# Kernel tuning notes

Hardware: AMD Instinct MI355X
Metric: run time of the kernel (lower is better)

Reference implementation:

```python
import jax, jax.numpy as jnp
import numpy as np

D_MODEL = 1024
NUM_HEADS = 16
HEAD_DIM = D_MODEL // NUM_HEADS
WINDOW = 16
DILATION = 3
SCALE = HEAD_DIM ** -0.5


def _linear(x, W, b):
    # torch nn.Linear: y = x @ W.T + b, W: [out, in]
    return x @ W.T + b


def _chunk_attention(x, Wq, bq, Wk, bk, Wv, bv, chunk):
    B, L, D = x.shape
    pad = (-L) % chunk
    if pad:
        x = jnp.pad(x, ((0, 0), (0, pad), (0, 0)))
    Lp = L + pad
    nC = Lp // chunk
    xr = x.reshape(B * nC, chunk, D)  # [BC, c, D]

    def heads(t):
        return t.reshape(B * nC, chunk, NUM_HEADS, HEAD_DIM).transpose(0, 2, 1, 3)

    q = heads(_linear(xr, Wq, bq))  # [BC, H, c, hd]
    k = heads(_linear(xr, Wk, bk))
    v = heads(_linear(xr, Wv, bv))
    attn = jax.nn.softmax(jnp.einsum('bhqd,bhkd->bhqk', q, k) * SCALE, axis=-1)
    out = jnp.einsum('bhqk,bhkd->bhqd', attn, v)  # [BC, H, c, hd]
    out = out.transpose(0, 2, 1, 3).reshape(B, Lp, D)
    return out[:, :L, :]


def setup_inputs() -> dict:
    key = jax.random.key(0)
    ks = jax.random.split(key, 9)
    s = 1.0 / np.sqrt(D_MODEL)
    x = jax.random.normal(ks[0], (4, 4096, D_MODEL), dtype=jnp.float32)
    def lin(kw, kb):
        W = jax.random.uniform(kw, (D_MODEL, D_MODEL), minval=-s, maxval=s, dtype=jnp.float32)
        b = jax.random.uniform(kb, (D_MODEL,), minval=-s, maxval=s, dtype=jnp.float32)
        return W, b
    Wq, bq = lin(ks[1], ks[2])
    Wk, bk = lin(ks[3], ks[4])
    Wv, bv = lin(ks[5], ks[6])
    Wo, bo = lin(ks[7], ks[8])
    return {"x": x, "Wq": Wq, "bq": bq, "Wk": Wk, "bk": bk,
            "Wv": Wv, "bv": bv, "Wo": Wo, "bo": bo}


def reference(x, Wq, bq, Wk, bk, Wv, bv, Wo, bo):
    B, L, D = x.shape
    # local windowed attention
    local_out = _chunk_attention(x, Wq, bq, Wk, bk, Wv, bv, WINDOW)
    # dilated (atrous) attention: stride-DILATION interleave via reshape/permute
    pad = (-L) % DILATION
    x_pad = jnp.pad(x, ((0, 0), (0, pad), (0, 0))) if pad else x
    Lp = L + pad
    xv = x_pad.reshape(B, Lp // DILATION, DILATION, D).transpose(0, 2, 1, 3)
    x_atrous = xv.reshape(B * DILATION, Lp // DILATION, D)
    a = _chunk_attention(x_atrous, Wq, bq, Wk, bk, Wv, bv, WINDOW)
    a = a.reshape(B, DILATION, Lp // DILATION, D).transpose(0, 2, 1, 3).reshape(B, Lp, D)
    atrous_out = a[:, :L, :]
    return _linear(local_out + atrous_out, Wo, bo)
```

## Files before the change

kernel.cpp:

```cpp
#include <hip/hip_runtime.h>
#include <hip/hip_bf16.h>
#include <stdint.h>

typedef unsigned short ushort_t;
typedef __attribute__((ext_vector_type(8))) short bf16x8;
typedef __attribute__((ext_vector_type(4))) float f32x4;

__device__ __forceinline__ ushort_t f2bf(float f) {
    uint32_t u = __builtin_bit_cast(uint32_t, f);
    u += 0x7FFF + ((u >> 16) & 1);
    return (ushort_t)(u >> 16);
}
__device__ __forceinline__ float bf2f(ushort_t h) {
    return __builtin_bit_cast(float, (uint32_t)h << 16);
}

__device__ __forceinline__ f32x4 mfma16(bf16x8 a, bf16x8 b, f32x4 c) {
    return __builtin_amdgcn_mfma_f32_16x16x32_bf16(a, b, c, 0, 0, 0);
}

#define GLL(g, l) __builtin_amdgcn_global_load_lds(                              \
    (const __attribute__((address_space(1))) void*)(g),                          \
    (__attribute__((address_space(3))) void*)(l), 16, 0, 0)

#define CFENCE asm volatile("" ::: "memory")
#define BARRIER do { CFENCE; __builtin_amdgcn_s_barrier(); CFENCE; } while (0)
#define PRIO1 __builtin_amdgcn_s_setprio(1)
#define PRIO0 __builtin_amdgcn_s_setprio(0)
#define VM4 asm volatile("s_waitcnt vmcnt(4)" ::: "memory")
#define VM0 asm volatile("s_waitcnt vmcnt(0)" ::: "memory")


__device__ __forceinline__ void cvt8(const float* s, ushort_t* d) {
    float4 a = ((const float4*)s)[0], b = ((const float4*)s)[1];
    union { bf16x8 v; ushort_t u[8]; } o;
    o.u[0] = f2bf(a.x); o.u[1] = f2bf(a.y); o.u[2] = f2bf(a.z); o.u[3] = f2bf(a.w);
    o.u[4] = f2bf(b.x); o.u[5] = f2bf(b.y); o.u[6] = f2bf(b.z); o.u[7] = f2bf(b.w);
    *(bf16x8*)d = o.v;
}

__global__ __launch_bounds__(256) void cvt_all(
    const float* __restrict__ x,
    const float* __restrict__ Wq, const float* __restrict__ Wk,
    const float* __restrict__ Wv, const float* __restrict__ Wo,
    const float* __restrict__ bq, const float* __restrict__ bk,
    const float* __restrict__ bv,
    ushort_t* __restrict__ xb, ushort_t* __restrict__ wqkv,
    float* __restrict__ bqkv)
{
    const int NX = 16384 * 1024 / 8;
    const int NW = 1024 * 1024 / 8;
    int i = blockIdx.x * 256 + threadIdx.x;
    if (i < NX) {
        cvt8(x + (size_t)i * 8, xb + (size_t)i * 8);
    } else if (i < NX + 4 * NW) {
        int j = i - NX;
        int w = j >> 17, off = j & (NW - 1);
        const float* s = (w == 0) ? Wq : (w == 1) ? Wk : (w == 2) ? Wv : Wo;
        cvt8(s + (size_t)off * 8, wqkv + (size_t)j * 8);
    } else if (i < NX + 4 * NW + 384) {
        int j = i - NX - 4 * NW;
        int w2 = j >> 7, off = j & 127;
        const float* s = (w2 == 0) ? bq : (w2 == 1) ? bk : bv;
        ((float4*)(bqkv + j * 8))[0] = ((const float4*)(s + off * 8))[0];
        ((float4*)(bqkv + j * 8))[1] = ((const float4*)(s + off * 8))[1];
    }
}


#define STGA(bq, kt) { _Pragma("unroll")                                         \
    for (int j = 0; j < 2; ++j) {                                                \
        int idx = j * 512 + tid; int row = idx >> 2, ch = idx & 3;               \
        GLL(A + (size_t)(m0 + row) * 1024 + (kt) * 32 + ((ch ^ (row & 3)) * 8),  \
            (char*)&As[bq][0] + (size_t)idx * 16);                               \
    } }
#define STGB(bq, kt) { _Pragma("unroll")                                         \
    for (int j = 0; j < 2; ++j) {                                                \
        int idx = j * 512 + tid; int row = idx >> 2, ch = idx & 3;               \
        GLL(B + (size_t)(n0 + row) * 1024 + (kt) * 32 + ((ch ^ (row & 3)) * 8),  \
            (char*)&Bs[bq][0] + (size_t)idx * 16);                               \
    } }

#define RD4(dst, bq, mibase) { _Pragma("unroll")                                 \
    for (int q = 0; q < 4; ++q)                                                  \
        dst[q] = *(const bf16x8*)&As[bq][(wm * 128 + ((mibase) + q) * 16 + ln)   \
                                        * 32 + cho]; }
#define RDB(dst, bq) { _Pragma("unroll")                                         \
    for (int q = 0; q < 4; ++q)                                                  \
        dst[q] = *(const bf16x8*)&Bs[bq][(wn * 64 + q * 16 + ln) * 32 + cho]; }

#define MFMA16(mibase, av, bv) { _Pragma("unroll")                               \
    for (int mi = 0; mi < 4; ++mi) _Pragma("unroll")                             \
        for (int ni = 0; ni < 4; ++ni)                                           \
            acc[(mibase) + mi][ni] =                                             \
                mfma16(av[mi], bv[ni], acc[(mibase) + mi][ni]); }

template<int MODE>
__global__ __launch_bounds__(512, 2) void gemm6(
    const ushort_t* __restrict__ A, const ushort_t* __restrict__ B,
    const float* __restrict__ bias, void* __restrict__ outp,
    int M, int NTN)
{
    __shared__ ushort_t As[4][256 * 32];
    __shared__ ushort_t Bs[4][256 * 32];
    const int NK = 32;

    const int bid = blockIdx.x;
    const int nwg = gridDim.x;
    const int q8 = nwg >> 3;
    const int swz = (bid & 7) * q8 + (bid >> 3);
    const int m0 = (swz / NTN) * 256;
    const int n0 = (swz % NTN) * 256;

    const int tid = threadIdx.x;
    const int wave = tid >> 6, lane = tid & 63;
    const int wm = wave >> 2, wn = wave & 3;
    const int lg = lane >> 4, ln = lane & 15;
    const int cho = (lg ^ (ln & 3)) * 8;

    f32x4 acc[8][4];
#pragma unroll
    for (int i2 = 0; i2 < 8; ++i2)
#pragma unroll
        for (int j2 = 0; j2 < 4; ++j2) acc[i2][j2] = (f32x4){0.f, 0.f, 0.f, 0.f};

    STGA(0, 0) STGB(0, 0)
    STGA(1, 1) STGB(1, 1)
    STGA(2, 2) STGB(2, 2)
    VM4;
    BARRIER;

    bf16x8 aE0[4], aE1[4], aO0[4], aO1[4], bE[4], bO[4];
    RD4(aE0, 0, 0) RDB(bE, 0)

    for (int it = 0; it < 16; ++it) {
        const int ke = 2 * it, ko = ke + 1;
        const int ce = (it & 1) << 1, co = ce | 1;
        const int s1 = (ke + 3) & 3;
        const int s2 = ce;
        const bool p1 = (ke + 3 < NK), p2 = (ko + 3 < NK);

        RD4(aE1, ce, 4)
        if (p1) STGA(s1, ke + 3)
        PRIO1; MFMA16(0, aE0, bE) PRIO0;

        RD4(aO0, co, 0) RDB(bO, co)
        if (p1) STGB(s1, ke + 3)
        PRIO1; MFMA16(4, aE1, bE) PRIO0;
        if (p1) { VM4; } else { VM0; }
        BARRIER;

        RD4(aO1, co, 4)
        if (p2) STGA(s2, ko + 3)
        PRIO1; MFMA16(0, aO0, bO) PRIO0;

        if (it + 1 < 16) { RD4(aE0, (ce + 2) & 3, 0) RDB(bE, (ce + 2) & 3) }
        if (p2) STGB(s2, ko + 3)
        PRIO1; MFMA16(4, aO1, bO) PRIO0;
        if (p2) { VM4; } else { VM0; }
        BARRIER;
    }

    float bval[4];
#pragma unroll
    for (int ni = 0; ni < 4; ++ni) bval[ni] = bias[n0 + wn * 64 + ni * 16 + ln];

    if (MODE == 0) {
        ushort_t* obase = (ushort_t*)outp + (size_t)(n0 >> 10) * ((size_t)M * 1024)
                          + (n0 & 1023) + wn * 64 + ln;
#pragma unroll
        for (int mi = 0; mi < 8; ++mi) {
#pragma unroll
            for (int r = 0; r < 4; ++r) {
                int m = m0 + wm * 128 + mi * 16 + lg * 4 + r;
                ushort_t* orow = obase + (size_t)m * 1024;
#pragma unroll
                for (int ni = 0; ni < 4; ++ni)
                    orow[ni * 16] = f2bf(acc[mi][ni][r] + bval[ni]);
            }
        }
    } else {
        float* obase = (float*)outp + n0 + wn * 64 + ln;
#pragma unroll
        for (int mi = 0; mi < 8; ++mi) {
#pragma unroll
            for (int r = 0; r < 4; ++r) {
                int m = m0 + wm * 128 + mi * 16 + lg * 4 + r;
                float* orow = obase + (size_t)m * 1024;
#pragma unroll
                for (int ni = 0; ni < 4; ++ni)
                    orow[ni * 16] = acc[mi][ni][r] + bval[ni];
            }
        }
    }
}


__device__ __forceinline__ bf16x8 bias8(const float* __restrict__ b, int off) {
    float4 f0 = *(const float4*)(b + off);
    float4 f1 = *(const float4*)(b + off + 4);
    union { bf16x8 v; ushort_t u[8]; } o;
    o.u[0] = f2bf(f0.x); o.u[1] = f2bf(f0.y); o.u[2] = f2bf(f0.z); o.u[3] = f2bf(f0.w);
    o.u[4] = f2bf(f1.x); o.u[5] = f2bf(f1.y); o.u[6] = f2bf(f1.z); o.u[7] = f2bf(f1.w);
    return o.v;
}


__global__ __launch_bounds__(256) void attn_local(
    const ushort_t* __restrict__ Q, const ushort_t* __restrict__ K,
    const ushort_t* __restrict__ V, ushort_t* __restrict__ S)
{
    const int wave = threadIdx.x >> 6, lane = threadIdx.x & 63;
    const int unit = blockIdx.x * 4 + wave;
    const int h = unit & 15;
    const int c = unit >> 4;
    const int g = lane >> 4, nn = lane & 15;
    __shared__ ushort_t lds_p[4][16 * 16];
    __shared__ ushort_t vt[4][64 * 16];

    const size_t rowb = (size_t)c * 16;
    size_t aoff = (rowb + nn) * 1024 + h * 64 + g * 8;
    bf16x8 qa0 = *(const bf16x8*)(Q + aoff);
    bf16x8 qa1 = *(const bf16x8*)(Q + aoff + 32);
    bf16x8 kb0 = *(const bf16x8*)(K + aoff);
    bf16x8 kb1 = *(const bf16x8*)(K + aoff + 32);

#pragma unroll
    for (int it = 0; it < 2; ++it) {
        int u = it * 64 + lane;
        int n = u >> 3, cc = u & 7;
        bf16x8 vv = *(const bf16x8*)(V + (rowb + n) * 1024 + h * 64 + cc * 8);
        union { bf16x8 v; ushort_t u8[8]; } vu; vu.v = vv;
#pragma unroll
        for (int j = 0; j < 8; ++j) vt[wave][(cc * 8 + j) * 16 + n] = vu.u8[j];
    }

    f32x4 sc = {0.f, 0.f, 0.f, 0.f};
    sc = mfma16(qa0, kb0, sc);
    sc = mfma16(qa1, kb1, sc);

#pragma unroll
    for (int r = 0; r < 4; ++r) {
        float s = sc[r] * 0.125f;
        float mx = s;
#pragma unroll
        for (int off = 1; off < 16; off <<= 1) mx = fmaxf(mx, __shfl_xor(mx, off, 64));
        float e = __expf(s - mx);
        float sm = e;
#pragma unroll
        for (int off = 1; off < 16; off <<= 1) sm += __shfl_xor(sm, off, 64);
        lds_p[wave][(g * 4 + r) * 16 + nn] = f2bf(e / sm);
    }
    CFENCE;

    bf16x8 zero8 = {};
    bf16x8 pa = (g < 2) ? *(const bf16x8*)&lds_p[wave][nn * 16 + g * 8] : zero8;
#pragma unroll
    for (int dt = 0; dt < 4; ++dt) {
        bf16x8 vb = (g < 2) ? *(const bf16x8*)&vt[wave][(dt * 16 + nn) * 16 + g * 8] : zero8;
        f32x4 o = mfma16(pa, vb, (f32x4){0.f, 0.f, 0.f, 0.f});
#pragma unroll
        for (int r = 0; r < 4; ++r) {
            size_t orow = rowb + g * 4 + r;
            S[orow * 1024 + h * 64 + dt * 16 + nn] = f2bf(o[r]);
        }
    }
}


__global__ __launch_bounds__(256) void attn_atrous(
    const ushort_t* __restrict__ Q, const ushort_t* __restrict__ K,
    const ushort_t* __restrict__ V,
    const float* __restrict__ bq, const float* __restrict__ bk,
    const float* __restrict__ bv, ushort_t* __restrict__ S)
{
    const int wave = threadIdx.x >> 6, lane = threadIdx.x & 63;
    const int unit = blockIdx.x * 4 + wave;
    const int h = unit & 15;
    const int tmp = unit >> 4;
    const int c = tmp % 86;
    const int sidx = tmp / 86;
    const int b = sidx / 3, dil = sidx % 3;
    const int g = lane >> 4, nn = lane & 15;
    __shared__ ushort_t lds_p[4][16 * 16];
    __shared__ ushort_t vt[4][64 * 16];

    const int dof = h * 64 + g * 8;
    const int p_n = 3 * (c * 16 + nn) + dil;
    bf16x8 qa0, qa1, kb0, kb1;
    if (p_n < 4096) {
        size_t o = ((size_t)b * 4096 + p_n) * 1024 + dof;
        qa0 = *(const bf16x8*)(Q + o);
        qa1 = *(const bf16x8*)(Q + o + 32);
        kb0 = *(const bf16x8*)(K + o);
        kb1 = *(const bf16x8*)(K + o + 32);
    } else {
        qa0 = bias8(bq, dof); qa1 = bias8(bq, dof + 32);
        kb0 = bias8(bk, dof); kb1 = bias8(bk, dof + 32);
    }

#pragma unroll
    for (int it = 0; it < 2; ++it) {
        int u = it * 64 + lane;
        int n = u >> 3, cc = u & 7;
        int p_v = 3 * (c * 16 + n) + dil;
        bf16x8 vv = (p_v < 4096)
            ? *(const bf16x8*)(V + ((size_t)b * 4096 + p_v) * 1024 + h * 64 + cc * 8)
            : bias8(bv, h * 64 + cc * 8);
        union { bf16x8 v; ushort_t u8[8]; } vu; vu.v = vv;
#pragma unroll
        for (int j = 0; j < 8; ++j) vt[wave][(cc * 8 + j) * 16 + n] = vu.u8[j];
    }

    f32x4 sc = {0.f, 0.f, 0.f, 0.f};
    sc = mfma16(qa0, kb0, sc);
    sc = mfma16(qa1, kb1, sc);

#pragma unroll
    for (int r = 0; r < 4; ++r) {
        float s = sc[r] * 0.125f;
        float mx = s;
#pragma unroll
        for (int off = 1; off < 16; off <<= 1) mx = fmaxf(mx, __shfl_xor(mx, off, 64));
        float e = __expf(s - mx);
        float sm = e;
#pragma unroll
        for (int off = 1; off < 16; off <<= 1) sm += __shfl_xor(sm, off, 64);
        lds_p[wave][(g * 4 + r) * 16 + nn] = f2bf(e / sm);
    }
    CFENCE;

    bf16x8 zero8 = {};
    bf16x8 pa = (g < 2) ? *(const bf16x8*)&lds_p[wave][nn * 16 + g * 8] : zero8;
#pragma unroll
    for (int dt = 0; dt < 4; ++dt) {
        bf16x8 vb = (g < 2) ? *(const bf16x8*)&vt[wave][(dt * 16 + nn) * 16 + g * 8] : zero8;
        f32x4 o = mfma16(pa, vb, (f32x4){0.f, 0.f, 0.f, 0.f});
#pragma unroll
        for (int r = 0; r < 4; ++r) {
            int p_q = 3 * (c * 16 + g * 4 + r) + dil;
            if (p_q < 4096) {
                size_t off = ((size_t)b * 4096 + p_q) * 1024 + h * 64 + dt * 16 + nn;
                S[off] = f2bf(bf2f(S[off]) + o[r]);
            }
        }
    }
}


extern "C" void kernel_launch(void* const* d_in, const int* in_sizes, int n_in,
                              void* d_out, int out_size, void* d_ws, size_t ws_size,
                              hipStream_t stream)
{
    const float* x  = (const float*)d_in[0];
    const float* Wq = (const float*)d_in[1];
    const float* bq = (const float*)d_in[2];
    const float* Wk = (const float*)d_in[3];
    const float* bk = (const float*)d_in[4];
    const float* Wv = (const float*)d_in[5];
    const float* bv = (const float*)d_in[6];
    const float* Wo = (const float*)d_in[7];
    const float* bo = (const float*)d_in[8];
    float* out = (float*)d_out;

    const size_t NT = 16384;
    ushort_t* xb   = (ushort_t*)d_ws;
    ushort_t* wqkv = xb + NT * 1024;
    ushort_t* wo   = wqkv + 3 * 1024 * 1024;
    ushort_t* Qb   = wo + 1024 * 1024;
    ushort_t* Kb   = Qb + NT * 1024;
    ushort_t* Vb   = Kb + NT * 1024;
    ushort_t* Sb   = Vb + NT * 1024;
    float*    bqkv = (float*)(Sb + NT * 1024);

    const int total_units = 2097152 + 4 * 131072 + 384;
    cvt_all<<<(total_units + 255) / 256, 256, 0, stream>>>(
        x, Wq, Wk, Wv, Wo, bq, bk, bv, xb, wqkv, bqkv);

    gemm6<0><<<768, 512, 0, stream>>>(xb, wqkv, bqkv, (void*)Qb, (int)NT, 12);

    attn_local <<<4096, 256, 0, stream>>>(Qb, Kb, Vb, Sb);
    attn_atrous<<<4128, 256, 0, stream>>>(Qb, Kb, Vb, bq, bk, bv, Sb);

    gemm6<1><<<256, 512, 0, stream>>>(Sb, wo, bo, (void*)out, (int)NT, 4);
}
```

Baseline: 344.9 us.

## Rework GEMM to K=64 double-buffered pipeline and fuse local+atrous attention bands

The GEMM moves from 32-wide K tiles with four stages to 64-wide K tiles with two buffers and an 8-chunk XOR swizzle. The loop is split into four phases, each loading one quarter of the next tile, and the launch bound drops to one block per CU. The two attention kernels are merged into one band kernel: each 48-token band computes its three local chunks and three dilated chunks together and sums them in LDS before a single bf16 store. This removes the read-modify-write of S and one launch. The risks are lower GEMM occupancy, more barriers per iteration, and fewer attention blocks that each loop over four heads with syncthreads.

```diff
diff --git a/kernel.cpp b/kernel.cpp
--- a/kernel.cpp
+++ b/kernel.cpp
@@ -27,7 +27,8 @@
 #define BARRIER do { CFENCE; __builtin_amdgcn_s_barrier(); CFENCE; } while (0)
 #define PRIO1 __builtin_amdgcn_s_setprio(1)
 #define PRIO0 __builtin_amdgcn_s_setprio(0)
-#define VM4 asm volatile("s_waitcnt vmcnt(4)" ::: "memory")
+#define LGKM0 asm volatile("s_waitcnt lgkmcnt(0)" ::: "memory")
+#define VM2 asm volatile("s_waitcnt vmcnt(2)" ::: "memory")
 #define VM0 asm volatile("s_waitcnt vmcnt(0)" ::: "memory")
 
 
@@ -68,42 +69,35 @@
 }
 
 
-#define STGA(bq, kt) { _Pragma("unroll")                                         \
+#define STG7(P, rb, dst, kt) { _Pragma("unroll")                                 \
     for (int j = 0; j < 2; ++j) {                                                \
-        int idx = j * 512 + tid; int row = idx >> 2, ch = idx & 3;               \
-        GLL(A + (size_t)(m0 + row) * 1024 + (kt) * 32 + ((ch ^ (row & 3)) * 8),  \
-            (char*)&As[bq][0] + (size_t)idx * 16);                               \
+        int idx = j * 512 + tid; int row = idx >> 3, ch = idx & 7;               \
+        GLL(P + (size_t)((rb) + row) * 1024 + (kt) * 64 + ((ch ^ (row & 7)) * 8),\
+            (char*)(dst) + (size_t)idx * 16);                                    \
     } }
-#define STGB(bq, kt) { _Pragma("unroll")                                         \
-    for (int j = 0; j < 2; ++j) {                                                \
-        int idx = j * 512 + tid; int row = idx >> 2, ch = idx & 3;               \
-        GLL(B + (size_t)(n0 + row) * 1024 + (kt) * 32 + ((ch ^ (row & 3)) * 8),  \
-            (char*)&Bs[bq][0] + (size_t)idx * 16);                               \
-    } }
-
-#define RD4(dst, bq, mibase) { _Pragma("unroll")                                 \
+
+#define RDA(dst, base, kki) { _Pragma("unroll")                                  \
     for (int q = 0; q < 4; ++q)                                                  \
-        dst[q] = *(const bf16x8*)&As[bq][(wm * 128 + ((mibase) + q) * 16 + ln)   \
-                                        * 32 + cho]; }
-#define RDB(dst, bq) { _Pragma("unroll")                                         \
+        dst[q] = *(const bf16x8*)&Ad[((base) + q) * 16 * 64 + ln * 64 + chA[kki]]; }
+#define RDB(kki) { _Pragma("unroll")                                             \
     for (int q = 0; q < 4; ++q)                                                  \
-        dst[q] = *(const bf16x8*)&Bs[bq][(wn * 64 + q * 16 + ln) * 32 + cho]; }
-
-#define MFMA16(mibase, av, bv) { _Pragma("unroll")                               \
+        bb[q] = *(const bf16x8*)&Bd[(q * 16 + ln) * 64 + chA[kki]]; }
+
+#define MFMA_P(mibase, areg) { _Pragma("unroll")                                 \
     for (int mi = 0; mi < 4; ++mi) _Pragma("unroll")                             \
         for (int ni = 0; ni < 4; ++ni)                                           \
             acc[(mibase) + mi][ni] =                                             \
-                mfma16(av[mi], bv[ni], acc[(mibase) + mi][ni]); }
+                mfma16(areg[mi], bb[ni], acc[(mibase) + mi][ni]); }
 
 template<int MODE>
-__global__ __launch_bounds__(512, 2) void gemm6(
+__global__ __launch_bounds__(512, 1) void gemm7(
     const ushort_t* __restrict__ A, const ushort_t* __restrict__ B,
     const float* __restrict__ bias, void* __restrict__ outp,
     int M, int NTN)
 {
-    __shared__ ushort_t As[4][256 * 32];
-    __shared__ ushort_t Bs[4][256 * 32];
-    const int NK = 32;
+    __shared__ ushort_t As[2][2][128 * 64];
+    __shared__ ushort_t Bs[2][2][128 * 64];
+    const int NK = 16;
 
     const int bid = blockIdx.x;
     const int nwg = gridDim.x;
@@ -116,7 +110,9 @@
     const int wave = tid >> 6, lane = tid & 63;
     const int wm = wave >> 2, wn = wave & 3;
     const int lg = lane >> 4, ln = lane & 15;
-    const int cho = (lg ^ (ln & 3)) * 8;
+    int chA[2];
+    chA[0] = ((0 * 4 + lg) ^ (ln & 7)) * 8;
+    chA[1] = ((1 * 4 + lg) ^ (ln & 7)) * 8;
 
     f32x4 acc[8][4];
 #pragma unroll
@@ -124,40 +120,45 @@
 #pragma unroll
         for (int j2 = 0; j2 < 4; ++j2) acc[i2][j2] = (f32x4){0.f, 0.f, 0.f, 0.f};
 
-    STGA(0, 0) STGB(0, 0)
-    STGA(1, 1) STGB(1, 1)
-    STGA(2, 2) STGB(2, 2)
-    VM4;
+    STG7(A, m0 + 0,   &As[0][0][0], 0)
+    STG7(A, m0 + 128, &As[0][1][0], 0)
+    STG7(B, n0 + 0,   &Bs[0][0][0], 0)
+    STG7(B, n0 + 128, &Bs[0][1][0], 0)
+    STG7(B, n0 + 0,   &Bs[1][0][0], 1)
+    VM2;
     BARRIER;
 
-    bf16x8 aE0[4], aE1[4], aO0[4], aO1[4], bE[4], bO[4];
-    RD4(aE0, 0, 0) RDB(bE, 0)
-
-    for (int it = 0; it < 16; ++it) {
-        const int ke = 2 * it, ko = ke + 1;
-        const int ce = (it & 1) << 1, co = ce | 1;
-        const int s1 = (ke + 3) & 3;
-        const int s2 = ce;
-        const bool p1 = (ke + 3 < NK), p2 = (ko + 3 < NK);
-
-        RD4(aE1, ce, 4)
-        if (p1) STGA(s1, ke + 3)
-        PRIO1; MFMA16(0, aE0, bE) PRIO0;
-
-        RD4(aO0, co, 0) RDB(bO, co)
-        if (p1) STGB(s1, ke + 3)
-        PRIO1; MFMA16(4, aE1, bE) PRIO0;
-        if (p1) { VM4; } else { VM0; }
+    bf16x8 a03[4], a47[4], bb[4];
+    for (int t = 0; t < NK; ++t) {
+        const int d = t & 1, o = d ^ 1;
+        const ushort_t* Ad = &As[d][wm][0];
+        const ushort_t* Bd = &Bs[d][wn >> 1][(wn & 1) * 64 * 64];
+        const bool p1 = (t + 1 < NK), p2 = (t + 2 < NK);
+
+        RDA(a03, 0, 0) RDB(0)
+        if (p1) STG7(B, n0 + 128, &Bs[o][1][0], t + 1)
+        BARRIER; LGKM0;
+        PRIO1; MFMA_P(0, a03) PRIO0;
         BARRIER;
 
-        RD4(aO1, co, 4)
-        if (p2) STGA(s2, ko + 3)
-        PRIO1; MFMA16(0, aO0, bO) PRIO0;
-
-        if (it + 1 < 16) { RD4(aE0, (ce + 2) & 3, 0) RDB(bE, (ce + 2) & 3) }
-        if (p2) STGB(s2, ko + 3)
-        PRIO1; MFMA16(4, aO1, bO) PRIO0;
-        if (p2) { VM4; } else { VM0; }
+        RDA(a47, 4, 0)
+        if (p1) STG7(A, m0 + 0, &As[o][0][0], t + 1)
+        BARRIER; LGKM0;
+        PRIO1; MFMA_P(4, a47) PRIO0;
+        BARRIER;
+
+        RDA(a03, 0, 1) RDB(1)
+        if (p1) STG7(A, m0 + 128, &As[o][1][0], t + 1)
+        BARRIER; LGKM0;
+        PRIO1; MFMA_P(0, a03) PRIO0;
+        BARRIER;
+
+        RDA(a47, 4, 1)
+        if (p2) STG7(B, n0 + 0, &Bs[d][0][0], t + 2)
+        if (p2)      { VM2; }
+        else if (p1) { VM0; }
+        BARRIER; LGKM0;
+        PRIO1; MFMA_P(4, a47) PRIO0;
         BARRIER;
     }
 
@@ -206,144 +207,114 @@
 }
 
 
-__global__ __launch_bounds__(256) void attn_local(
-    const ushort_t* __restrict__ Q, const ushort_t* __restrict__ K,
-    const ushort_t* __restrict__ V, ushort_t* __restrict__ S)
-{
-    const int wave = threadIdx.x >> 6, lane = threadIdx.x & 63;
-    const int unit = blockIdx.x * 4 + wave;
-    const int h = unit & 15;
-    const int c = unit >> 4;
-    const int g = lane >> 4, nn = lane & 15;
-    __shared__ ushort_t lds_p[4][16 * 16];
-    __shared__ ushort_t vt[4][64 * 16];
-
-    const size_t rowb = (size_t)c * 16;
-    size_t aoff = (rowb + nn) * 1024 + h * 64 + g * 8;
-    bf16x8 qa0 = *(const bf16x8*)(Q + aoff);
-    bf16x8 qa1 = *(const bf16x8*)(Q + aoff + 32);
-    bf16x8 kb0 = *(const bf16x8*)(K + aoff);
-    bf16x8 kb1 = *(const bf16x8*)(K + aoff + 32);
-
-#pragma unroll
-    for (int it = 0; it < 2; ++it) {
-        int u = it * 64 + lane;
-        int n = u >> 3, cc = u & 7;
-        bf16x8 vv = *(const bf16x8*)(V + (rowb + n) * 1024 + h * 64 + cc * 8);
-        union { bf16x8 v; ushort_t u8[8]; } vu; vu.v = vv;
-#pragma unroll
-        for (int j = 0; j < 8; ++j) vt[wave][(cc * 8 + j) * 16 + n] = vu.u8[j];
-    }
-
-    f32x4 sc = {0.f, 0.f, 0.f, 0.f};
-    sc = mfma16(qa0, kb0, sc);
-    sc = mfma16(qa1, kb1, sc);
-
-#pragma unroll
-    for (int r = 0; r < 4; ++r) {
-        float s = sc[r] * 0.125f;
-        float mx = s;
-#pragma unroll
-        for (int off = 1; off < 16; off <<= 1) mx = fmaxf(mx, __shfl_xor(mx, off, 64));
-        float e = __expf(s - mx);
-        float sm = e;
-#pragma unroll
-        for (int off = 1; off < 16; off <<= 1) sm += __shfl_xor(sm, off, 64);
-        lds_p[wave][(g * 4 + r) * 16 + nn] = f2bf(e / sm);
-    }
-    CFENCE;
-
-    bf16x8 zero8 = {};
-    bf16x8 pa = (g < 2) ? *(const bf16x8*)&lds_p[wave][nn * 16 + g * 8] : zero8;
-#pragma unroll
-    for (int dt = 0; dt < 4; ++dt) {
-        bf16x8 vb = (g < 2) ? *(const bf16x8*)&vt[wave][(dt * 16 + nn) * 16 + g * 8] : zero8;
-        f32x4 o = mfma16(pa, vb, (f32x4){0.f, 0.f, 0.f, 0.f});
-#pragma unroll
-        for (int r = 0; r < 4; ++r) {
-            size_t orow = rowb + g * 4 + r;
-            S[orow * 1024 + h * 64 + dt * 16 + nn] = f2bf(o[r]);
-        }
-    }
-}
-
-
-__global__ __launch_bounds__(256) void attn_atrous(
+__global__ __launch_bounds__(384) void attn_band(
     const ushort_t* __restrict__ Q, const ushort_t* __restrict__ K,
     const ushort_t* __restrict__ V,
     const float* __restrict__ bq, const float* __restrict__ bk,
     const float* __restrict__ bv, ushort_t* __restrict__ S)
 {
     const int wave = threadIdx.x >> 6, lane = threadIdx.x & 63;
-    const int unit = blockIdx.x * 4 + wave;
-    const int h = unit & 15;
-    const int tmp = unit >> 4;
-    const int c = tmp % 86;
-    const int sidx = tmp / 86;
-    const int b = sidx / 3, dil = sidx % 3;
     const int g = lane >> 4, nn = lane & 15;
-    __shared__ ushort_t lds_p[4][16 * 16];
-    __shared__ ushort_t vt[4][64 * 16];
-
-    const int dof = h * 64 + g * 8;
-    const int p_n = 3 * (c * 16 + nn) + dil;
-    bf16x8 qa0, qa1, kb0, kb1;
-    if (p_n < 4096) {
-        size_t o = ((size_t)b * 4096 + p_n) * 1024 + dof;
-        qa0 = *(const bf16x8*)(Q + o);
-        qa1 = *(const bf16x8*)(Q + o + 32);
-        kb0 = *(const bf16x8*)(K + o);
-        kb1 = *(const bf16x8*)(K + o + 32);
-    } else {
-        qa0 = bias8(bq, dof); qa1 = bias8(bq, dof + 32);
-        kb0 = bias8(bk, dof); kb1 = bias8(bk, dof + 32);
-    }
-
-#pragma unroll
-    for (int it = 0; it < 2; ++it) {
-        int u = it * 64 + lane;
-        int n = u >> 3, cc = u & 7;
-        int p_v = 3 * (c * 16 + n) + dil;
-        bf16x8 vv = (p_v < 4096)
-            ? *(const bf16x8*)(V + ((size_t)b * 4096 + p_v) * 1024 + h * 64 + cc * 8)
-            : bias8(bv, h * 64 + cc * 8);
-        union { bf16x8 v; ushort_t u8[8]; } vu; vu.v = vv;
-#pragma unroll
-        for (int j = 0; j < 8; ++j) vt[wave][(cc * 8 + j) * 16 + n] = vu.u8[j];
-    }
-
-    f32x4 sc = {0.f, 0.f, 0.f, 0.f};
-    sc = mfma16(qa0, kb0, sc);
-    sc = mfma16(qa1, kb1, sc);
-
-#pragma unroll
-    for (int r = 0; r < 4; ++r) {
-        float s = sc[r] * 0.125f;
-        float mx = s;
-#pragma unroll
-        for (int off = 1; off < 16; off <<= 1) mx = fmaxf(mx, __shfl_xor(mx, off, 64));
-        float e = __expf(s - mx);
-        float sm = e;
-#pragma unroll
-        for (int off = 1; off < 16; off <<= 1) sm += __shfl_xor(sm, off, 64);
-        lds_p[wave][(g * 4 + r) * 16 + nn] = f2bf(e / sm);
-    }
-    CFENCE;
-
-    bf16x8 zero8 = {};
-    bf16x8 pa = (g < 2) ? *(const bf16x8*)&lds_p[wave][nn * 16 + g * 8] : zero8;
-#pragma unroll
-    for (int dt = 0; dt < 4; ++dt) {
-        bf16x8 vb = (g < 2) ? *(const bf16x8*)&vt[wave][(dt * 16 + nn) * 16 + g * 8] : zero8;
-        f32x4 o = mfma16(pa, vb, (f32x4){0.f, 0.f, 0.f, 0.f});
+    const int bid = blockIdx.x;
+    const int hq = bid & 3;
+    const int t2 = bid >> 2;
+    const int band = t2 % 86;
+    const int b = t2 / 86;
+
+    __shared__ float Sacc[48 * 64];
+    __shared__ ushort_t vt[6][64 * 16];
+    __shared__ ushort_t lds_p[6][16 * 16];
+
+    const bool is_local = (wave < 3);
+    const int dil = wave - 3;
+    const int tb = band * 48;
+    const size_t batch0 = (size_t)b * 4096;
+
+    for (int hi = 0; hi < 4; ++hi) {
+        const int h = hq * 4 + hi;
+        const int dof = h * 64 + g * 8;
+
+        int tok_n = is_local ? (tb + wave * 16 + nn) : (tb + 3 * nn + dil);
+        bf16x8 qa0, qa1, kb0, kb1;
+        if (is_local || tok_n < 4096) {
+            size_t off = (batch0 + tok_n) * 1024 + dof;
+            qa0 = *(const bf16x8*)(Q + off);
+            qa1 = *(const bf16x8*)(Q + off + 32);
+            kb0 = *(const bf16x8*)(K + off);
+            kb1 = *(const bf16x8*)(K + off + 32);
+        } else {
+            qa0 = bias8(bq, dof); qa1 = bias8(bq, dof + 32);
+            kb0 = bias8(bk, dof); kb1 = bias8(bk, dof + 32);
+        }
+
+#pragma unroll
+        for (int it = 0; it < 2; ++it) {
+            int u = it * 64 + lane;
+            int n = u >> 3, cc = u & 7;
+            int tok_v = is_local ? (tb + wave * 16 + n) : (tb + 3 * n + dil);
+            bf16x8 vv = (is_local || tok_v < 4096)
+                ? *(const bf16x8*)(V + (batch0 + tok_v) * 1024 + h * 64 + cc * 8)
+                : bias8(bv, h * 64 + cc * 8);
+            union { bf16x8 v; ushort_t u8[8]; } vu; vu.v = vv;
+#pragma unroll
+            for (int j = 0; j < 8; ++j) vt[wave][(cc * 8 + j) * 16 + n] = vu.u8[j];
+        }
+
+        f32x4 sc = {0.f, 0.f, 0.f, 0.f};
+        sc = mfma16(qa0, kb0, sc);
+        sc = mfma16(qa1, kb1, sc);
 #pragma unroll
         for (int r = 0; r < 4; ++r) {
-            int p_q = 3 * (c * 16 + g * 4 + r) + dil;
-            if (p_q < 4096) {
-                size_t off = ((size_t)b * 4096 + p_q) * 1024 + h * 64 + dt * 16 + nn;
-                S[off] = f2bf(bf2f(S[off]) + o[r]);
+            float s = sc[r] * 0.125f;
+            float mx = s;
+#pragma unroll
+            for (int off = 1; off < 16; off <<= 1) mx = fmaxf(mx, __shfl_xor(mx, off, 64));
+            float e = __expf(s - mx);
+            float sm = e;
+#pragma unroll
+            for (int off = 1; off < 16; off <<= 1) sm += __shfl_xor(sm, off, 64);
+            lds_p[wave][(g * 4 + r) * 16 + nn] = f2bf(e / sm);
+        }
+        CFENCE;
+
+        bf16x8 zero8 = {};
+        bf16x8 pa = (g < 2) ? *(const bf16x8*)&lds_p[wave][nn * 16 + g * 8] : zero8;
+        f32x4 o[4];
+#pragma unroll
+        for (int dt = 0; dt < 4; ++dt) {
+            bf16x8 vb = (g < 2) ? *(const bf16x8*)&vt[wave][(dt * 16 + nn) * 16 + g * 8] : zero8;
+            o[dt] = mfma16(pa, vb, (f32x4){0.f, 0.f, 0.f, 0.f});
+        }
+
+        if (is_local) {
+#pragma unroll
+            for (int dt = 0; dt < 4; ++dt)
+#pragma unroll
+                for (int r = 0; r < 4; ++r)
+                    Sacc[(wave * 16 + g * 4 + r) * 64 + dt * 16 + nn] = o[dt][r];
+        }
+        __syncthreads();
+        if (!is_local) {
+#pragma unroll
+            for (int dt = 0; dt < 4; ++dt)
+#pragma unroll
+                for (int r = 0; r < 4; ++r)
+                    Sacc[(3 * (g * 4 + r) + dil) * 64 + dt * 16 + nn] += o[dt][r];
+        }
+        __syncthreads();
+
+        {
+            int row = threadIdx.x >> 3, cg = threadIdx.x & 7;
+            int tok = tb + row;
+            if (tok < 4096) {
+                const float* src = &Sacc[row * 64 + cg * 8];
+                union { bf16x8 v; ushort_t u8[8]; } ov;
+#pragma unroll
+                for (int j = 0; j < 8; ++j) ov.u8[j] = f2bf(src[j]);
+                *(bf16x8*)(S + (batch0 + tok) * 1024 + h * 64 + cg * 8) = ov.v;
             }
         }
+        __syncthreads();
     }
 }
 
@@ -377,10 +348,9 @@
     cvt_all<<<(total_units + 255) / 256, 256, 0, stream>>>(
         x, Wq, Wk, Wv, Wo, bq, bk, bv, xb, wqkv, bqkv);
 
-    gemm6<0><<<768, 512, 0, stream>>>(xb, wqkv, bqkv, (void*)Qb, (int)NT, 12);
-
-    attn_local <<<4096, 256, 0, stream>>>(Qb, Kb, Vb, Sb);
-    attn_atrous<<<4128, 256, 0, stream>>>(Qb, Kb, Vb, bq, bk, bv, Sb);
-
-    gemm6<1><<<256, 512, 0, stream>>>(Sb, wo, bo, (void*)out, (int)NT, 4);
-}
+    gemm7<0><<<768, 512, 0, stream>>>(xb, wqkv, bqkv, (void*)Qb, (int)NT, 12);
+
+    attn_band<<<4 * 86 * 4, 384, 0, stream>>>(Qb, Kb, Vb, bq, bk, bv, Sb);
+
+    gemm7<1><<<256, 512, 0, stream>>>(Sb, wo, bo, (void*)out, (int)NT, 4);
+}
```

New measurement: 348.3 us. About the same (+1.0%).
